# Optimization experiments

Hardware: AMD Instinct MI355X
Metric: run time of the kernel (lower is better)

## Reference

```python
import jax, jax.numpy as jnp
import numpy as np

B, S, D, H = 2, 2048, 1024, 16
DK = D // H

def setup_inputs() -> dict:
    key = jax.random.key(0)
    ks = jax.random.split(key, 11)
    scale = 1.0 / np.sqrt(D)
    inp = {
        'query': jax.random.normal(ks[0], (B, S, D), jnp.float32),
        'key':   jax.random.normal(ks[1], (B, S, D), jnp.float32),
        'value': jax.random.normal(ks[2], (B, S, D), jnp.float32),
        'wq': jax.random.normal(ks[3], (D, D), jnp.float32) * scale,
        'bq': jax.random.normal(ks[4], (D,), jnp.float32) * 0.01,
        'wk': jax.random.normal(ks[5], (D, D), jnp.float32) * scale,
        'bk': jax.random.normal(ks[6], (D,), jnp.float32) * 0.01,
        'wv': jax.random.normal(ks[7], (D, D), jnp.float32) * scale,
        'bv': jax.random.normal(ks[8], (D,), jnp.float32) * 0.01,
        'wo': jax.random.normal(ks[9], (D, D), jnp.float32) * scale,
        'bo': jax.random.normal(ks[10], (D,), jnp.float32) * 0.01,
    }
    return inp

def reference(query, key, value, wq, bq, wk, bk, wv, bv, wo, bo):
    nb = query.shape[0]
    # projections: torch nn.Linear computes x @ W^T + b; here weights stored as (in,out)
    def proj(x, w, b):
        return (x @ w + b).reshape(nb, -1, H, DK).transpose(0, 2, 1, 3)  # [B,H,S,dk]
    q = proj(query, wq, bq)
    k = proj(key, wk, bk)
    v = proj(value, wv, bv)
    scores = jnp.einsum('bhqd,bhkd->bhqk', q, k) / jnp.sqrt(jnp.float32(DK))
    p = jax.nn.softmax(scores, axis=-1)  # dropout p=0 (eval)
    x = jnp.einsum('bhqk,bhkd->bhqd', p, v)
    x = x.transpose(0, 2, 1, 3).reshape(nb, -1, H * DK)
    return x @ wo + bo
```

## Files before the change

kernel.cpp:

```cpp
#include <hip/hip_runtime.h>


typedef __attribute__((ext_vector_type(8))) __bf16 bf16x8;
typedef __attribute__((ext_vector_type(4))) __bf16 bf16x4;
typedef __attribute__((ext_vector_type(8))) float f32x8;
typedef __attribute__((ext_vector_type(4))) float f32x4;

#define MFMA16 __builtin_amdgcn_mfma_f32_16x16x32_bf16

union Bf8 { bf16x8 v; __bf16 e[8]; };

__device__ inline f32x4 zero4() { f32x4 z; z[0]=z[1]=z[2]=z[3]=0.f; return z; }

__global__ __launch_bounds__(256) void prep_w(
        const float* __restrict__ w0, const float* __restrict__ w1,
        const float* __restrict__ w2, const float* __restrict__ w3,
        __bf16* __restrict__ wt) {
    const float* src = blockIdx.z == 0 ? w0 : blockIdx.z == 1 ? w1 :
                       blockIdx.z == 2 ? w2 : w3;
    __bf16* dst = wt + (size_t)blockIdx.z * 1048576;
    __shared__ float tile[32][33];
    const int t = threadIdx.x;
    const int tc = t & 31, tr = t >> 5;
    const int r0 = blockIdx.y * 32, c0 = blockIdx.x * 32;
#pragma unroll
    for (int i = 0; i < 4; i++) {
        int r = tr + i * 8;
        tile[r][tc] = src[(size_t)(r0 + r) * 1024 + c0 + tc];
    }
    __syncthreads();
#pragma unroll
    for (int i = 0; i < 4; i++) {
        int r = tr + i * 8;
        dst[(size_t)(c0 + r) * 1024 + r0 + tc] = (__bf16)tile[tc][r];
    }
}

__global__ __launch_bounds__(256) void prep_x(
        const float* __restrict__ x0, const float* __restrict__ x1,
        const float* __restrict__ x2, __bf16* __restrict__ xb) {
    const float* src = blockIdx.y == 0 ? x0 : blockIdx.y == 1 ? x1 : x2;
    __bf16* dst = xb + (size_t)blockIdx.y * 4194304;
    size_t g = ((size_t)blockIdx.x * 256 + threadIdx.x) * 8;
    f32x8 a = *(const f32x8*)&src[g];
    Bf8 tmp;
#pragma unroll
    for (int j = 0; j < 8; j++) tmp.e[j] = (__bf16)a[j];
    *(bf16x8*)&dst[g] = tmp.v;
}

template <int MODE, bool AF32, typename OutT>
__device__ inline void gemm_core(const void* __restrict__ Av,
                                 const __bf16* __restrict__ Bt,
                                 const float* __restrict__ bias,
                                 OutT* __restrict__ out) {
    __shared__ __bf16 As[128 * 72];
    __shared__ __bf16 Bs[128 * 72];
    const int t = threadIdx.x;
    const int wave = t >> 6, lane = t & 63, lm = lane & 15, quad = lane >> 4;
    const int m0 = blockIdx.y * 128, n0 = blockIdx.x * 128;
    const int wm = (wave >> 1) * 64, wn = (wave & 1) * 64;

    f32x4 acc[4][4];
#pragma unroll
    for (int i = 0; i < 4; i++)
#pragma unroll
        for (int j = 0; j < 4; j++) acc[i][j] = zero4();

    for (int k0 = 0; k0 < 1024; k0 += 64) {
#pragma unroll
        for (int i = 0; i < 4; i++) {
            int c = i * 256 + t;
            int row = c >> 3, c8 = c & 7;
            size_t aoff = (size_t)(m0 + row) * 1024 + k0 + c8 * 8;
            if (AF32) {
                f32x8 a = *(const f32x8*)&((const float*)Av)[aoff];
                Bf8 tmp;
#pragma unroll
                for (int j = 0; j < 8; j++) tmp.e[j] = (__bf16)a[j];
                *(bf16x8*)&As[row * 72 + c8 * 8] = tmp.v;
            } else {
                *(bf16x8*)&As[row * 72 + c8 * 8] =
                    *(const bf16x8*)&((const __bf16*)Av)[aoff];
            }
            *(bf16x8*)&Bs[row * 72 + c8 * 8] =
                *(const bf16x8*)&Bt[(size_t)(n0 + row) * 1024 + k0 + c8 * 8];
        }
        __syncthreads();
#pragma unroll
        for (int ks = 0; ks < 2; ks++) {
            bf16x8 af[4], bfr[4];
#pragma unroll
            for (int mt = 0; mt < 4; mt++)
                af[mt] = *(const bf16x8*)&As[(wm + mt * 16 + lm) * 72 + ks * 32 + quad * 8];
#pragma unroll
            for (int nt = 0; nt < 4; nt++)
                bfr[nt] = *(const bf16x8*)&Bs[(wn + nt * 16 + lm) * 72 + ks * 32 + quad * 8];
#pragma unroll
            for (int mt = 0; mt < 4; mt++)
#pragma unroll
                for (int nt = 0; nt < 4; nt++)
                    acc[mt][nt] = MFMA16(af[mt], bfr[nt], acc[mt][nt], 0, 0, 0);
        }
        __syncthreads();
    }

    float bv4[4];
#pragma unroll
    for (int nt = 0; nt < 4; nt++) bv4[nt] = bias[n0 + wn + nt * 16 + lm];

#pragma unroll
    for (int mt = 0; mt < 4; mt++) {
#pragma unroll
        for (int r = 0; r < 4; r++) {
            int row = m0 + wm + mt * 16 + quad * 4 + r;
#pragma unroll
            for (int nt = 0; nt < 4; nt++) {
                int col = n0 + wn + nt * 16 + lm;
                float val = acc[mt][nt][r] + bv4[nt];
                size_t idx;
                if (MODE == 0) {
                    idx = (size_t)row * 1024 + col;
                } else {
                    int b = row >> 11, s = row & 2047, hh = col >> 6, dk = col & 63;
                    if (MODE == 1)
                        idx = (size_t)(b * 16 + hh) * 131072 + (size_t)s * 64 + dk;
                    else
                        idx = (size_t)(b * 16 + hh) * 131072 + (size_t)dk * 2048 + s;
                }
                out[idx] = (OutT)val;
            }
        }
    }
}

template <bool AF32>
__global__ __launch_bounds__(256) void proj_kernel(
        const void* __restrict__ q, const void* __restrict__ k,
        const void* __restrict__ v, const __bf16* __restrict__ WT,
        const float* __restrict__ bq, const float* __restrict__ bk,
        const float* __restrict__ bv,
        __bf16* __restrict__ Q, __bf16* __restrict__ K, __bf16* __restrict__ Vt) {
    int z = blockIdx.z;
    if (z == 0)      gemm_core<1, AF32, __bf16>(q, WT,           bq, Q);
    else if (z == 1) gemm_core<1, AF32, __bf16>(k, WT + 1048576, bk, K);
    else             gemm_core<2, AF32, __bf16>(v, WT + 2097152, bv, Vt);
}

__global__ __launch_bounds__(256) void out_proj_kernel(
        const __bf16* __restrict__ A, const __bf16* __restrict__ Bt,
        const float* __restrict__ bias, float* __restrict__ out) {
    gemm_core<0, false, float>(A, Bt, bias, out);
}

__global__ __launch_bounds__(256, 2) void attn_kernel(
        const __bf16* __restrict__ Q, const __bf16* __restrict__ K,
        const __bf16* __restrict__ Vt, __bf16* __restrict__ O) {
    __shared__ __bf16 Ks[128 * 72];
    __shared__ __bf16 Vs[64 * 136];
    __shared__ __bf16 Ps[4 * 32 * 136];
    const int t = threadIdx.x;
    const int wave = t >> 6, lane = t & 63, lm = lane & 15, quad = lane >> 4;
    const int q0 = blockIdx.x * 128;
    const int bh = blockIdx.y;
    const size_t base = (size_t)bh * 131072;

    bf16x8 bq[2][2];
    {
        int qrow = q0 + wave * 32;
#pragma unroll
        for (int nt = 0; nt < 2; nt++)
#pragma unroll
            for (int ks = 0; ks < 2; ks++)
                bq[nt][ks] = *(const bf16x8*)
                    &Q[base + (size_t)(qrow + nt * 16 + lm) * 64 + ks * 32 + quad * 8];
    }

    float m_run[2], l_run[2];
#pragma unroll
    for (int n = 0; n < 2; n++) { m_run[n] = -1e30f; l_run[n] = 0.f; }
    f32x4 o_acc[4][2];
#pragma unroll
    for (int mt = 0; mt < 4; mt++)
#pragma unroll
        for (int n = 0; n < 2; n++) o_acc[mt][n] = zero4();

    __bf16* Pw = &Ps[wave * 32 * 136];

    for (int kv0 = 0; kv0 < 2048; kv0 += 128) {
#pragma unroll
        for (int i = 0; i < 4; i++) {
            int c = i * 256 + t;
            {
                int row = c >> 3, c8 = c & 7;
                *(bf16x8*)&Ks[row * 72 + c8 * 8] =
                    *(const bf16x8*)&K[base + (size_t)(kv0 + row) * 64 + c8 * 8];
            }
            {
                int row = c >> 4, c16 = c & 15;
                *(bf16x8*)&Vs[row * 136 + c16 * 8] =
                    *(const bf16x8*)&Vt[base + (size_t)row * 2048 + kv0 + c16 * 8];
            }
        }
        __syncthreads();

        f32x4 sc[8][2];
#pragma unroll
        for (int mt = 0; mt < 8; mt++) {
            sc[mt][0] = zero4();
            sc[mt][1] = zero4();
#pragma unroll
            for (int ks = 0; ks < 2; ks++) {
                bf16x8 ak = *(const bf16x8*)&Ks[(mt * 16 + lm) * 72 + ks * 32 + quad * 8];
                sc[mt][0] = MFMA16(ak, bq[0][ks], sc[mt][0], 0, 0, 0);
                sc[mt][1] = MFMA16(ak, bq[1][ks], sc[mt][1], 0, 0, 0);
            }
        }

#pragma unroll
        for (int nt = 0; nt < 2; nt++) {
            float mx = -1e30f;
#pragma unroll
            for (int mt = 0; mt < 8; mt++)
#pragma unroll
                for (int r = 0; r < 4; r++) {
                    sc[mt][nt][r] *= 0.125f;
                    mx = fmaxf(mx, sc[mt][nt][r]);
                }
            mx = fmaxf(mx, __shfl_xor(mx, 16));
            mx = fmaxf(mx, __shfl_xor(mx, 32));
            float mn = fmaxf(m_run[nt], mx);
            float alpha = __expf(m_run[nt] - mn);
            m_run[nt] = mn;
            float su = 0.f;
#pragma unroll
            for (int mt = 0; mt < 8; mt++)
#pragma unroll
                for (int r = 0; r < 4; r++) {
                    float p = __expf(sc[mt][nt][r] - mn);
                    sc[mt][nt][r] = p;
                    su += p;
                }
            su += __shfl_xor(su, 16);
            su += __shfl_xor(su, 32);
            l_run[nt] = l_run[nt] * alpha + su;
#pragma unroll
            for (int mt = 0; mt < 4; mt++)
#pragma unroll
                for (int r = 0; r < 4; r++) o_acc[mt][nt][r] *= alpha;
        }

#pragma unroll
        for (int nt = 0; nt < 2; nt++)
#pragma unroll
            for (int mt = 0; mt < 8; mt++) {
                bf16x4 pk;
#pragma unroll
                for (int r = 0; r < 4; r++) pk[r] = (__bf16)sc[mt][nt][r];
                *(bf16x4*)&Pw[(nt * 16 + lm) * 136 + mt * 16 + quad * 4] = pk;
            }
        __asm__ volatile("" ::: "memory");

#pragma unroll
        for (int ks = 0; ks < 4; ks++) {
            bf16x8 bp[2];
#pragma unroll
            for (int nt = 0; nt < 2; nt++)
                bp[nt] = *(const bf16x8*)&Pw[(nt * 16 + lm) * 136 + ks * 32 + quad * 8];
#pragma unroll
            for (int mt = 0; mt < 4; mt++) {
                bf16x8 av = *(const bf16x8*)&Vs[(mt * 16 + lm) * 136 + ks * 32 + quad * 8];
                o_acc[mt][0] = MFMA16(av, bp[0], o_acc[mt][0], 0, 0, 0);
                o_acc[mt][1] = MFMA16(av, bp[1], o_acc[mt][1], 0, 0, 0);
            }
        }
        __syncthreads();
    }

#pragma unroll
    for (int nt = 0; nt < 2; nt++) {
        float inv = 1.f / l_run[nt];
#pragma unroll
        for (int mt = 0; mt < 4; mt++) {
            bf16x4 pk;
#pragma unroll
            for (int r = 0; r < 4; r++) pk[r] = (__bf16)(o_acc[mt][nt][r] * inv);
            *(bf16x4*)&Pw[(nt * 16 + lm) * 136 + mt * 16 + quad * 4] = pk;
        }
    }
    __asm__ volatile("" ::: "memory");
    {
        const int b = bh >> 4, h = bh & 15;
        int ql = lane >> 1, half = lane & 1;
        int srow = q0 + wave * 32 + ql;
#pragma unroll
        for (int j = 0; j < 4; j++) {
            bf16x8 v = *(const bf16x8*)&Pw[ql * 136 + half * 32 + j * 8];
            *(bf16x8*)&O[(size_t)(b * 2048 + srow) * 1024 + h * 64 + half * 32 + j * 8] = v;
        }
    }
}

extern "C" void kernel_launch(void* const* d_in, const int* in_sizes, int n_in,
                              void* d_out, int out_size, void* d_ws, size_t ws_size,
                              hipStream_t stream) {
    if (ws_size < ((size_t)40 << 20)) return;

    const float* query = (const float*)d_in[0];
    const float* key_  = (const float*)d_in[1];
    const float* value = (const float*)d_in[2];
    const float* wq = (const float*)d_in[3];
    const float* bq = (const float*)d_in[4];
    const float* wk = (const float*)d_in[5];
    const float* bk = (const float*)d_in[6];
    const float* wv = (const float*)d_in[7];
    const float* bv = (const float*)d_in[8];
    const float* wo = (const float*)d_in[9];
    const float* bo = (const float*)d_in[10];
    float* out = (float*)d_out;

    char* ws = (char*)d_ws;
    const bool big = ws_size >= ((size_t)72 << 20);
    __bf16* WT  = (__bf16*)(ws);
    __bf16* Xb  = (__bf16*)(ws + ((size_t)8 << 20));
    size_t o0 = big ? ((size_t)32 << 20) : ((size_t)8 << 20);
    __bf16* Qw  = (__bf16*)(ws + o0);
    __bf16* Kw  = (__bf16*)(ws + o0 + ((size_t)8 << 20));
    __bf16* Vtw = (__bf16*)(ws + o0 + ((size_t)16 << 20));
    __bf16* Ow  = (__bf16*)(ws + o0 + ((size_t)24 << 20));

    prep_w<<<dim3(32, 32, 4), dim3(256), 0, stream>>>(wq, wk, wv, wo, WT);
    if (big) {
        prep_x<<<dim3(2048, 3), dim3(256), 0, stream>>>(query, key_, value, Xb);
        proj_kernel<false><<<dim3(8, 32, 3), dim3(256), 0, stream>>>(
            Xb, Xb + 4194304, Xb + 8388608, WT, bq, bk, bv, Qw, Kw, Vtw);
    } else {
        proj_kernel<true><<<dim3(8, 32, 3), dim3(256), 0, stream>>>(
            query, key_, value, WT, bq, bk, bv, Qw, Kw, Vtw);
    }
    attn_kernel<<<dim3(16, 32), dim3(256), 0, stream>>>(Qw, Kw, Vtw, Ow);
    out_proj_kernel<<<dim3(8, 32), dim3(256), 0, stream>>>(
        Ow, WT + 3 * 1048576, bo, out);
}
```

Before: 255.0 us.

## Use direct global-to-LDS loads with XOR swizzle, drop input prepass, shrink attention LDS

Replaces padded LDS tiles with XOR-swizzled 64/128-wide layouts filled by global_load_lds for the bf16 GEMM B operand, the out-projection A operand and the attention K/V tiles. The separate fp32-to-bf16 input conversion kernel is removed, so the projection always converts fp32 inputs inline. The V projection now writes its transposed output through an LDS staging buffer with vector stores, and the 1/sqrt(dk) scale is folded into the Q projection. Attention processes P one 16-row half at a time to shrink the P buffer and raises launch bounds to 3 blocks per SM for occupancy. The risk is register pressure from the higher occupancy target and slower projection loads, since inline conversion makes each fp32 A tile be re-read across all N tiles.

```diff
diff --git a/kernel.cpp b/kernel.cpp
--- a/kernel.cpp
+++ b/kernel.cpp
@@ -12,15 +12,20 @@
 
 __device__ inline f32x4 zero4() { f32x4 z; z[0]=z[1]=z[2]=z[3]=0.f; return z; }
 
+__device__ inline void load_lds16(const void* g, void* l) {
+    __builtin_amdgcn_global_load_lds(
+        (const __attribute__((address_space(1))) unsigned int*)g,
+        (__attribute__((address_space(3))) unsigned int*)l, 16, 0, 0);
+}
+
 __global__ __launch_bounds__(256) void prep_w(
         const float* __restrict__ w0, const float* __restrict__ w1,
         const float* __restrict__ w2, const float* __restrict__ w3,
         __bf16* __restrict__ wt) {
-    const float* src = blockIdx.z == 0 ? w0 : blockIdx.z == 1 ? w1 :
-                       blockIdx.z == 2 ? w2 : w3;
-    __bf16* dst = wt + (size_t)blockIdx.z * 1048576;
+    const int z = blockIdx.z, t = threadIdx.x;
+    const float* src = z == 0 ? w0 : z == 1 ? w1 : z == 2 ? w2 : w3;
+    __bf16* dst = wt + (size_t)z * 1048576;
     __shared__ float tile[32][33];
-    const int t = threadIdx.x;
     const int tc = t & 31, tr = t >> 5;
     const int r0 = blockIdx.y * 32, c0 = blockIdx.x * 32;
 #pragma unroll
@@ -36,26 +41,14 @@
     }
 }
 
-__global__ __launch_bounds__(256) void prep_x(
-        const float* __restrict__ x0, const float* __restrict__ x1,
-        const float* __restrict__ x2, __bf16* __restrict__ xb) {
-    const float* src = blockIdx.y == 0 ? x0 : blockIdx.y == 1 ? x1 : x2;
-    __bf16* dst = xb + (size_t)blockIdx.y * 4194304;
-    size_t g = ((size_t)blockIdx.x * 256 + threadIdx.x) * 8;
-    f32x8 a = *(const f32x8*)&src[g];
-    Bf8 tmp;
-#pragma unroll
-    for (int j = 0; j < 8; j++) tmp.e[j] = (__bf16)a[j];
-    *(bf16x8*)&dst[g] = tmp.v;
-}
-
 template <int MODE, bool AF32, typename OutT>
-__device__ inline void gemm_core(const void* __restrict__ Av,
-                                 const __bf16* __restrict__ Bt,
-                                 const float* __restrict__ bias,
-                                 OutT* __restrict__ out) {
-    __shared__ __bf16 As[128 * 72];
-    __shared__ __bf16 Bs[128 * 72];
+__device__ inline void gemm_fast_core(const void* __restrict__ Av,
+                                      const __bf16* __restrict__ Bt,
+                                      const float* __restrict__ bias,
+                                      OutT* __restrict__ out, float scale) {
+    __shared__ __bf16 smem[16384];
+    __bf16* As = smem;
+    __bf16* Bs = smem + 8192;
     const int t = threadIdx.x;
     const int wave = t >> 6, lane = t & 63, lm = lane & 15, quad = lane >> 4;
     const int m0 = blockIdx.y * 128, n0 = blockIdx.x * 128;
@@ -70,21 +63,21 @@
     for (int k0 = 0; k0 < 1024; k0 += 64) {
 #pragma unroll
         for (int i = 0; i < 4; i++) {
-            int c = i * 256 + t;
-            int row = c >> 3, c8 = c & 7;
-            size_t aoff = (size_t)(m0 + row) * 1024 + k0 + c8 * 8;
+            int s = i * 256 + t;
+            int row = s >> 3, cb = (s & 7) ^ (row & 7);
+            size_t goff = (size_t)row * 1024 + k0 + cb * 8;
             if (AF32) {
-                f32x8 a = *(const f32x8*)&((const float*)Av)[aoff];
+                f32x8 a = *(const f32x8*)&((const float*)Av)[(size_t)m0 * 1024 + goff];
                 Bf8 tmp;
 #pragma unroll
                 for (int j = 0; j < 8; j++) tmp.e[j] = (__bf16)a[j];
-                *(bf16x8*)&As[row * 72 + c8 * 8] = tmp.v;
+                *(bf16x8*)&As[(size_t)s * 8] = tmp.v;
             } else {
-                *(bf16x8*)&As[row * 72 + c8 * 8] =
-                    *(const bf16x8*)&((const __bf16*)Av)[aoff];
-            }
-            *(bf16x8*)&Bs[row * 72 + c8 * 8] =
-                *(const bf16x8*)&Bt[(size_t)(n0 + row) * 1024 + k0 + c8 * 8];
+                load_lds16(&((const __bf16*)Av)[(size_t)m0 * 1024 + goff],
+                           &As[(size_t)(i * 256 + wave * 64) * 8]);
+            }
+            load_lds16(&Bt[(size_t)n0 * 1024 + goff],
+                       &Bs[(size_t)(i * 256 + wave * 64) * 8]);
         }
         __syncthreads();
 #pragma unroll
@@ -92,10 +85,12 @@
             bf16x8 af[4], bfr[4];
 #pragma unroll
             for (int mt = 0; mt < 4; mt++)
-                af[mt] = *(const bf16x8*)&As[(wm + mt * 16 + lm) * 72 + ks * 32 + quad * 8];
+                af[mt] = *(const bf16x8*)&As[(wm + mt * 16 + lm) * 64 +
+                                             (((ks * 4 + quad) ^ (lm & 7)) * 8)];
 #pragma unroll
             for (int nt = 0; nt < 4; nt++)
-                bfr[nt] = *(const bf16x8*)&Bs[(wn + nt * 16 + lm) * 72 + ks * 32 + quad * 8];
+                bfr[nt] = *(const bf16x8*)&Bs[(wn + nt * 16 + lm) * 64 +
+                                              (((ks * 4 + quad) ^ (lm & 7)) * 8)];
 #pragma unroll
             for (int mt = 0; mt < 4; mt++)
 #pragma unroll
@@ -109,56 +104,82 @@
 #pragma unroll
     for (int nt = 0; nt < 4; nt++) bv4[nt] = bias[n0 + wn + nt * 16 + lm];
 
-#pragma unroll
-    for (int mt = 0; mt < 4; mt++) {
-#pragma unroll
-        for (int r = 0; r < 4; r++) {
-            int row = m0 + wm + mt * 16 + quad * 4 + r;
-#pragma unroll
-            for (int nt = 0; nt < 4; nt++) {
-                int col = n0 + wn + nt * 16 + lm;
-                float val = acc[mt][nt][r] + bv4[nt];
-                size_t idx;
-                if (MODE == 0) {
-                    idx = (size_t)row * 1024 + col;
-                } else {
-                    int b = row >> 11, s = row & 2047, hh = col >> 6, dk = col & 63;
-                    if (MODE == 1)
+    if (MODE == 2) {
+#pragma unroll
+        for (int mt = 0; mt < 4; mt++)
+#pragma unroll
+            for (int r = 0; r < 4; r++) {
+                int rr = wm + mt * 16 + quad * 4 + r;
+#pragma unroll
+                for (int nt = 0; nt < 4; nt++) {
+                    int c = wn + nt * 16 + lm;
+                    smem[c * 128 + (rr ^ (8 * (c & 15)))] =
+                        (__bf16)((acc[mt][nt][r] + bv4[nt]) * scale);
+                }
+            }
+        __syncthreads();
+        const int b = m0 >> 11;
+#pragma unroll
+        for (int it = 0; it < 8; it++) {
+            int g = it * 256 + t;
+            int c = g >> 4, gr = g & 15;
+            bf16x8 v = *(const bf16x8*)&smem[c * 128 + ((gr * 8) ^ (8 * (c & 15)))];
+            int col = n0 + c, hh = col >> 6, dk = col & 63;
+            int sglob = (m0 & 2047) + gr * 8;
+            size_t idx = (size_t)(b * 16 + hh) * 131072 + (size_t)dk * 2048 + sglob;
+            *(bf16x8*)&out[idx] = v;
+        }
+    } else {
+#pragma unroll
+        for (int mt = 0; mt < 4; mt++) {
+#pragma unroll
+            for (int r = 0; r < 4; r++) {
+                int row = m0 + wm + mt * 16 + quad * 4 + r;
+#pragma unroll
+                for (int nt = 0; nt < 4; nt++) {
+                    int col = n0 + wn + nt * 16 + lm;
+                    float val = (acc[mt][nt][r] + bv4[nt]) * scale;
+                    size_t idx;
+                    if (MODE == 0) {
+                        idx = (size_t)row * 1024 + col;
+                    } else {
+                        int b = row >> 11, s = row & 2047, hh = col >> 6, dk = col & 63;
                         idx = (size_t)(b * 16 + hh) * 131072 + (size_t)s * 64 + dk;
-                    else
-                        idx = (size_t)(b * 16 + hh) * 131072 + (size_t)dk * 2048 + s;
+                    }
+                    out[idx] = (OutT)val;
                 }
-                out[idx] = (OutT)val;
-            }
-        }
-    }
-}
-
-template <bool AF32>
-__global__ __launch_bounds__(256) void proj_kernel(
-        const void* __restrict__ q, const void* __restrict__ k,
-        const void* __restrict__ v, const __bf16* __restrict__ WT,
+            }
+        }
+    }
+}
+
+__global__ __launch_bounds__(256) void proj_fast3(
+        const float* __restrict__ q, const float* __restrict__ k,
+        const float* __restrict__ v, const __bf16* __restrict__ WT,
         const float* __restrict__ bq, const float* __restrict__ bk,
         const float* __restrict__ bv,
         __bf16* __restrict__ Q, __bf16* __restrict__ K, __bf16* __restrict__ Vt) {
     int z = blockIdx.z;
-    if (z == 0)      gemm_core<1, AF32, __bf16>(q, WT,           bq, Q);
-    else if (z == 1) gemm_core<1, AF32, __bf16>(k, WT + 1048576, bk, K);
-    else             gemm_core<2, AF32, __bf16>(v, WT + 2097152, bv, Vt);
-}
-
-__global__ __launch_bounds__(256) void out_proj_kernel(
+    if (z == 0)
+        gemm_fast_core<1, true, __bf16>(q, WT, bq, Q, 0.125f);
+    else if (z == 1)
+        gemm_fast_core<1, true, __bf16>(k, WT + 1048576, bk, K, 1.f);
+    else
+        gemm_fast_core<2, true, __bf16>(v, WT + 2097152, bv, Vt, 1.f);
+}
+
+__global__ __launch_bounds__(256) void out_proj_fast(
         const __bf16* __restrict__ A, const __bf16* __restrict__ Bt,
         const float* __restrict__ bias, float* __restrict__ out) {
-    gemm_core<0, false, float>(A, Bt, bias, out);
-}
-
-__global__ __launch_bounds__(256, 2) void attn_kernel(
+    gemm_fast_core<0, false, float>(A, Bt, bias, out, 1.f);
+}
+
+__global__ __launch_bounds__(256, 3) void attn_kernel(
         const __bf16* __restrict__ Q, const __bf16* __restrict__ K,
         const __bf16* __restrict__ Vt, __bf16* __restrict__ O) {
-    __shared__ __bf16 Ks[128 * 72];
-    __shared__ __bf16 Vs[64 * 136];
-    __shared__ __bf16 Ps[4 * 32 * 136];
+    __shared__ __bf16 Ks[8192];
+    __shared__ __bf16 Vs[8192];
+    __shared__ __bf16 Ps[4 * 16 * 136];
     const int t = threadIdx.x;
     const int wave = t >> 6, lane = t & 63, lm = lane & 15, quad = lane >> 4;
     const int q0 = blockIdx.x * 128;
@@ -185,21 +206,21 @@
 #pragma unroll
         for (int n = 0; n < 2; n++) o_acc[mt][n] = zero4();
 
-    __bf16* Pw = &Ps[wave * 32 * 136];
+    __bf16* Pw = &Ps[wave * 16 * 136];
 
     for (int kv0 = 0; kv0 < 2048; kv0 += 128) {
 #pragma unroll
         for (int i = 0; i < 4; i++) {
-            int c = i * 256 + t;
+            int s = i * 256 + t;
             {
-                int row = c >> 3, c8 = c & 7;
-                *(bf16x8*)&Ks[row * 72 + c8 * 8] =
-                    *(const bf16x8*)&K[base + (size_t)(kv0 + row) * 64 + c8 * 8];
+                int row = s >> 3, cb = (s & 7) ^ (row & 7);
+                load_lds16(&K[base + (size_t)(kv0 + row) * 64 + cb * 8],
+                           &Ks[(size_t)(i * 256 + wave * 64) * 8]);
             }
             {
-                int row = c >> 4, c16 = c & 15;
-                *(bf16x8*)&Vs[row * 136 + c16 * 8] =
-                    *(const bf16x8*)&Vt[base + (size_t)row * 2048 + kv0 + c16 * 8];
+                int row = s >> 4, cb = (s & 15) ^ (row & 15);
+                load_lds16(&Vt[base + (size_t)row * 2048 + kv0 + cb * 8],
+                           &Vs[(size_t)(i * 256 + wave * 64) * 8]);
             }
         }
         __syncthreads();
@@ -211,7 +232,8 @@
             sc[mt][1] = zero4();
 #pragma unroll
             for (int ks = 0; ks < 2; ks++) {
-                bf16x8 ak = *(const bf16x8*)&Ks[(mt * 16 + lm) * 72 + ks * 32 + quad * 8];
+                bf16x8 ak = *(const bf16x8*)&Ks[(mt * 16 + lm) * 64 +
+                                                (((ks * 4 + quad) ^ (lm & 7)) * 8)];
                 sc[mt][0] = MFMA16(ak, bq[0][ks], sc[mt][0], 0, 0, 0);
                 sc[mt][1] = MFMA16(ak, bq[1][ks], sc[mt][1], 0, 0, 0);
             }
@@ -223,10 +245,7 @@
 #pragma unroll
             for (int mt = 0; mt < 8; mt++)
 #pragma unroll
-                for (int r = 0; r < 4; r++) {
-                    sc[mt][nt][r] *= 0.125f;
-                    mx = fmaxf(mx, sc[mt][nt][r]);
-                }
+                for (int r = 0; r < 4; r++) mx = fmaxf(mx, sc[mt][nt][r]);
             mx = fmaxf(mx, __shfl_xor(mx, 16));
             mx = fmaxf(mx, __shfl_xor(mx, 32));
             float mn = fmaxf(m_run[nt], mx);
@@ -248,35 +267,32 @@
             for (int mt = 0; mt < 4; mt++)
 #pragma unroll
                 for (int r = 0; r < 4; r++) o_acc[mt][nt][r] *= alpha;
-        }
-
-#pragma unroll
-        for (int nt = 0; nt < 2; nt++)
+
 #pragma unroll
             for (int mt = 0; mt < 8; mt++) {
                 bf16x4 pk;
 #pragma unroll
                 for (int r = 0; r < 4; r++) pk[r] = (__bf16)sc[mt][nt][r];
-                *(bf16x4*)&Pw[(nt * 16 + lm) * 136 + mt * 16 + quad * 4] = pk;
-            }
-        __asm__ volatile("" ::: "memory");
-
-#pragma unroll
-        for (int ks = 0; ks < 4; ks++) {
-            bf16x8 bp[2];
-#pragma unroll
-            for (int nt = 0; nt < 2; nt++)
-                bp[nt] = *(const bf16x8*)&Pw[(nt * 16 + lm) * 136 + ks * 32 + quad * 8];
-#pragma unroll
-            for (int mt = 0; mt < 4; mt++) {
-                bf16x8 av = *(const bf16x8*)&Vs[(mt * 16 + lm) * 136 + ks * 32 + quad * 8];
-                o_acc[mt][0] = MFMA16(av, bp[0], o_acc[mt][0], 0, 0, 0);
-                o_acc[mt][1] = MFMA16(av, bp[1], o_acc[mt][1], 0, 0, 0);
-            }
-        }
-        __syncthreads();
-    }
-
+                *(bf16x4*)&Pw[lm * 136 + mt * 16 + quad * 4] = pk;
+            }
+            __asm__ volatile("" ::: "memory");
+
+#pragma unroll
+            for (int ks = 0; ks < 4; ks++) {
+                bf16x8 bp = *(const bf16x8*)&Pw[lm * 136 + ks * 32 + quad * 8];
+#pragma unroll
+                for (int mt = 0; mt < 4; mt++) {
+                    bf16x8 av = *(const bf16x8*)&Vs[(mt * 16 + lm) * 128 +
+                                                    (((ks * 4 + quad) ^ lm) * 8)];
+                    o_acc[mt][nt] = MFMA16(av, bp, o_acc[mt][nt], 0, 0, 0);
+                }
+            }
+            __asm__ volatile("" ::: "memory");
+        }
+        __syncthreads();
+    }
+
+    const int b = bh >> 4, h = bh & 15;
 #pragma unroll
     for (int nt = 0; nt < 2; nt++) {
         float inv = 1.f / l_run[nt];
@@ -285,19 +301,19 @@
             bf16x4 pk;
 #pragma unroll
             for (int r = 0; r < 4; r++) pk[r] = (__bf16)(o_acc[mt][nt][r] * inv);
-            *(bf16x4*)&Pw[(nt * 16 + lm) * 136 + mt * 16 + quad * 4] = pk;
-        }
-    }
-    __asm__ volatile("" ::: "memory");
-    {
-        const int b = bh >> 4, h = bh & 15;
-        int ql = lane >> 1, half = lane & 1;
-        int srow = q0 + wave * 32 + ql;
-#pragma unroll
-        for (int j = 0; j < 4; j++) {
-            bf16x8 v = *(const bf16x8*)&Pw[ql * 136 + half * 32 + j * 8];
-            *(bf16x8*)&O[(size_t)(b * 2048 + srow) * 1024 + h * 64 + half * 32 + j * 8] = v;
-        }
+            *(bf16x4*)&Pw[lm * 136 + mt * 16 + quad * 4] = pk;
+        }
+        __asm__ volatile("" ::: "memory");
+        {
+            int row = lane >> 2, colb = (lane & 3) * 16;
+            int srow = q0 + wave * 32 + nt * 16 + row;
+#pragma unroll
+            for (int j = 0; j < 2; j++) {
+                bf16x8 v = *(const bf16x8*)&Pw[row * 136 + colb + j * 8];
+                *(bf16x8*)&O[(size_t)(b * 2048 + srow) * 1024 + h * 64 + colb + j * 8] = v;
+            }
+        }
+        __asm__ volatile("" ::: "memory");
     }
 }
 
@@ -320,25 +336,16 @@
     float* out = (float*)d_out;
 
     char* ws = (char*)d_ws;
-    const bool big = ws_size >= ((size_t)72 << 20);
     __bf16* WT  = (__bf16*)(ws);
-    __bf16* Xb  = (__bf16*)(ws + ((size_t)8 << 20));
-    size_t o0 = big ? ((size_t)32 << 20) : ((size_t)8 << 20);
-    __bf16* Qw  = (__bf16*)(ws + o0);
-    __bf16* Kw  = (__bf16*)(ws + o0 + ((size_t)8 << 20));
-    __bf16* Vtw = (__bf16*)(ws + o0 + ((size_t)16 << 20));
-    __bf16* Ow  = (__bf16*)(ws + o0 + ((size_t)24 << 20));
+    __bf16* Qw  = (__bf16*)(ws + ((size_t)8  << 20));
+    __bf16* Kw  = (__bf16*)(ws + ((size_t)16 << 20));
+    __bf16* Vtw = (__bf16*)(ws + ((size_t)24 << 20));
+    __bf16* Ow  = (__bf16*)(ws + ((size_t)32 << 20));
 
     prep_w<<<dim3(32, 32, 4), dim3(256), 0, stream>>>(wq, wk, wv, wo, WT);
-    if (big) {
-        prep_x<<<dim3(2048, 3), dim3(256), 0, stream>>>(query, key_, value, Xb);
-        proj_kernel<false><<<dim3(8, 32, 3), dim3(256), 0, stream>>>(
-            Xb, Xb + 4194304, Xb + 8388608, WT, bq, bk, bv, Qw, Kw, Vtw);
-    } else {
-        proj_kernel<true><<<dim3(8, 32, 3), dim3(256), 0, stream>>>(
-            query, key_, value, WT, bq, bk, bv, Qw, Kw, Vtw);
-    }
+    proj_fast3<<<dim3(8, 32, 3), dim3(256), 0, stream>>>(
+        query, key_, value, WT, bq, bk, bv, Qw, Kw, Vtw);
     attn_kernel<<<dim3(16, 32), dim3(256), 0, stream>>>(Qw, Kw, Vtw, Ow);
-    out_proj_kernel<<<dim3(8, 32), dim3(256), 0, stream>>>(
+    out_proj_fast<<<dim3(8, 32), dim3(256), 0, stream>>>(
         Ow, WT + 3 * 1048576, bo, out);
 }
```

Result: slower. 308.1 us (+20.8%).
